# Performance work log

Measured on AMD Instinct MI355X. Metric: run time of the kernel, lower is better.

Reference implementation:

```python
import math
import jax, jax.numpy as jnp
import numpy as np

BATCH = 2048
LATENT = 64
BETA = 6.0
LOG_2PI = math.log(2.0 * math.pi)


def setup_inputs() -> dict:
    key = jax.random.key(0)
    k1, k2, k3 = jax.random.split(key, 3)
    z = jax.random.normal(k1, (BATCH, LATENT), dtype=jnp.float32)
    z_mean = jax.random.normal(k2, (BATCH, LATENT), dtype=jnp.float32)
    z_logvar = jax.random.normal(k3, (BATCH, LATENT), dtype=jnp.float32)
    return {"z": z, "z_mean": z_mean, "z_logvar": z_logvar}


def _gaussian_log_density(samples, mean, log_var):
    # elementwise Gaussian log-density, broadcasts to [B, B, L]
    inv_sigma = jnp.exp(-log_var)
    tmp = samples - mean
    return -0.5 * (tmp * tmp * inv_sigma + log_var + LOG_2PI)


def _total_correlation(z, z_mean, z_logvar):
    # log q(z_i | x_j) per-dim: [B, B, L]
    log_qz_prob = _gaussian_log_density(z[:, None, :], z_mean[None, :, :], z_logvar[None, :, :])
    # log prod_l (1/B) sum_j q(z_l | x_j)  (constants dropped as in original)
    log_qz_product = jnp.sum(jax.scipy.special.logsumexp(log_qz_prob, axis=1), axis=1)  # [B]
    # log (1/B) sum_j q(z | x_j)
    log_qz = jax.scipy.special.logsumexp(jnp.sum(log_qz_prob, axis=2), axis=1)  # [B]
    return jnp.mean(log_qz - log_qz_product)


def _gaussian_kl(z_mean, z_logvar):
    # standard KL(q(z|x) || N(0, I)), mean over batch
    return 0.5 * jnp.mean(
        jnp.sum(jnp.square(z_mean) + jnp.exp(z_logvar) - z_logvar - 1.0, axis=1)
    )


def reference(z, z_mean, z_logvar):
    kl_loss = _gaussian_kl(z_mean, z_logvar)
    tc = (BETA - 1.0) * _total_correlation(z, z_mean, z_logvar)
    return tc + kl_loss
```

## Files before the change

kernel.cpp:

```cpp
#include <hip/hip_runtime.h>
#include <math.h>

#define BATCH 2048
#define LATENT 64
#define LOG_2PI 1.8378770664093453f
#define BETA_M1 5.0f
#define LN2 0.69314718055994530942f
#define C2 (-0.72134752044448170368f)
#define EXP2F __builtin_amdgcn_exp2f
#define LOG2F __builtin_amdgcn_logf

#define OFF_VT   0
#define OFF_TCE  (128*BATCH)
#define OFF_UP   (OFF_TCE + 64*BATCH)
#define OFF_CE   (OFF_UP + 128*BATCH)
#define OFF_KLP  (OFF_CE + BATCH)
#define OFF_RMP  (OFF_KLP + BATCH)
#define OFF_RSP  (OFF_RMP + 8*BATCH)
#define OFF_PART (OFF_RSP + 8*BATCH)
#define OFF_SM   (OFF_PART + 16)

__global__ __launch_bounds__(256) void precompute_kernel(const float* __restrict__ z,
                                                         const float* __restrict__ zm,
                                                         const float* __restrict__ zlv,
                                                         float* __restrict__ ws) {
    __shared__ float Tz[16][65], Tm[16][65], Tlv[16][65];
    __shared__ float CEp[16][16], KLp[16][16];
    int t = threadIdx.x, lane = t & 63, w = t >> 6;
    int j0 = blockIdx.x * 16;

    #pragma unroll
    for (int p = 0; p < 4; ++p) {
        int jr = p * 4 + w;
        int idx = (j0 + jr) * LATENT + lane;
        Tz[jr][lane]  = z[idx];
        Tm[jr][lane]  = zm[idx];
        Tlv[jr][lane] = zlv[idx];
    }
    if (blockIdx.x == 0 && t < 16) ws[OFF_PART + t] = 0.0f;
    __syncthreads();

    int jl = t & 15, lg = t >> 4;
    int j = j0 + jl;
    float ce_acc = 0.0f, kl_acc = 0.0f;
    #pragma unroll
    for (int q = 0; q < 4; ++q) {
        int l = q * 16 + lg;
        float zv = Tz[jl][l];
        float m  = Tm[jl][l];
        float lv = Tlv[jl][l];
        float iv  = __expf(-lv);
        float civ = C2 * iv;
        float miv = m * iv;
        float cmv = C2 * miv;
        float cev = C2 * fmaf(m, miv, lv + LOG_2PI);
        ws[OFF_VT  + (2*l)   * BATCH + j] = civ;
        ws[OFF_VT  + (2*l+1) * BATCH + j] = cmv;
        ws[OFF_TCE + l       * BATCH + j] = cev;
        ws[OFF_UP  + (2*l)   * BATCH + j] = zv * zv;
        ws[OFF_UP  + (2*l+1) * BATCH + j] = -2.0f * zv;
        ce_acc += cev;
        kl_acc += fmaf(m, m, __expf(lv)) - lv - 1.0f;
    }
    CEp[lg][jl] = ce_acc;
    KLp[lg][jl] = kl_acc;
    __syncthreads();
    if (t < 16) {
        float ce = 0.0f, kl = 0.0f;
        #pragma unroll
        for (int g = 0; g < 16; ++g) { ce += CEp[g][t]; kl += KLp[g][t]; }
        ws[OFF_CE  + j0 + t] = ce;
        ws[OFF_KLP + j0 + t] = kl;
    }
}


__device__ __forceinline__ void dim_part(float* __restrict__ ws, int bx, int t,
                                         float (*Dred)[64]) {
    int l = bx >> 5, ic = bx & 31;
    int i0 = ic * 64;
    int ig = t & 7, js = t >> 3;
    int ib = i0 + ig * 8;

    const float* __restrict__ up0 = ws + OFF_UP + (2*l)   * BATCH + ib;
    const float* __restrict__ up1 = ws + OFF_UP + (2*l+1) * BATCH + ib;
    float4 za = *(const float4*)(up0);
    float4 zb = *(const float4*)(up0 + 4);
    float4 na = *(const float4*)(up1);
    float4 nb = *(const float4*)(up1 + 4);
    float z2[8] = {za.x, za.y, za.z, za.w, zb.x, zb.y, zb.z, zb.w};
    float n2[8] = {na.x, na.y, na.z, na.w, nb.x, nb.y, nb.z, nb.w};

    const float4* __restrict__ pc4 = (const float4*)(ws + OFF_VT  + (2*l)   * BATCH + js * 64);
    const float4* __restrict__ pm4 = (const float4*)(ws + OFF_VT  + (2*l+1) * BATCH + js * 64);
    const float4* __restrict__ pe4 = (const float4*)(ws + OFF_TCE + l       * BATCH + js * 64);

    float s[8] = {0.f, 0.f, 0.f, 0.f, 0.f, 0.f, 0.f, 0.f};

    #pragma unroll 4
    for (int q = 0; q < 16; ++q) {
        float4 cc = pc4[q], mm = pm4[q], ee = pe4[q];
        #pragma unroll
        for (int k = 0; k < 8; ++k) {
            s[k] += EXP2F(fmaf(z2[k], cc.x, fmaf(n2[k], mm.x, ee.x)));
            s[k] += EXP2F(fmaf(z2[k], cc.y, fmaf(n2[k], mm.y, ee.y)));
            s[k] += EXP2F(fmaf(z2[k], cc.z, fmaf(n2[k], mm.z, ee.z)));
            s[k] += EXP2F(fmaf(z2[k], cc.w, fmaf(n2[k], mm.w, ee.w)));
        }
    }

    #pragma unroll
    for (int off = 8; off < 64; off <<= 1) {
        #pragma unroll
        for (int k = 0; k < 8; ++k)
            s[k] += __shfl_xor(s[k], off, 64);
    }
    int lane = t & 63, w = t >> 6;
    if (lane < 8) {
        #pragma unroll
        for (int k = 0; k < 8; ++k) Dred[w][lane * 8 + k] = s[k];
    }
    __syncthreads();
    if (t < 64) {
        float v = Dred[0][t] + Dred[1][t] + Dred[2][t] + Dred[3][t];
        ws[OFF_SM + l * BATCH + i0 + t] = v;
    }
    __syncthreads();
}

__device__ __forceinline__ void row_part(float* __restrict__ ws, int bx, int t,
                                         float* __restrict__ Ups,
                                         float (*RMs)[4], float (*RSs)[4]) {
    int ig = bx >> 3, jq = bx & 7;
    int i0 = ig * 8;
    int j  = jq * 256 + t;

    #pragma unroll
    for (int p = 0; p < 4; ++p) {
        int f = t + 256 * p;
        Ups[f] = ws[OFF_UP + (f >> 3) * BATCH + i0 + (f & 7)];
    }
    __syncthreads();

    float r[8];
    #pragma unroll
    for (int i = 0; i < 8; ++i) r[i] = 0.0f;

    const float* __restrict__ Vt = ws + OFF_VT;
    for (int l = 0; l < LATENT; ++l) {
        float v0 = Vt[(2*l)   * BATCH + j];
        float v1 = Vt[(2*l+1) * BATCH + j];
        const float* __restrict__ ua = Ups + (2*l)   * 8;
        const float* __restrict__ ub = Ups + (2*l+1) * 8;
        #pragma unroll
        for (int i = 0; i < 8; ++i)
            r[i] = fmaf(ua[i], v0, fmaf(ub[i], v1, r[i]));
    }

    float ce = ws[OFF_CE + j];
    int lane = t & 63, w = t >> 6;
    #pragma unroll
    for (int i = 0; i < 8; ++i) {
        float M = r[i] + ce;
        float S = 1.0f;
        #pragma unroll
        for (int off = 32; off > 0; off >>= 1) {
            float Mo = __shfl_xor(M, off, 64);
            float So = __shfl_xor(S, off, 64);
            float mn = fmaxf(M, Mo);
            S = S * EXP2F(M - mn) + So * EXP2F(Mo - mn);
            M = mn;
        }
        if (lane == 0) { RMs[i][w] = M; RSs[i][w] = S; }
    }
    __syncthreads();
    if (t < 8) {
        float M = RMs[t][0], S = RSs[t][0];
        #pragma unroll
        for (int w2 = 1; w2 < 4; ++w2) {
            float Mo = RMs[t][w2], So = RSs[t][w2];
            float mn = fmaxf(M, Mo);
            S = S * EXP2F(M - mn) + So * EXP2F(Mo - mn);
            M = mn;
        }
        ws[OFF_RMP + jq * BATCH + i0 + t] = M;
        ws[OFF_RSP + jq * BATCH + i0 + t] = S;
    }
    __syncthreads();
}

__global__ __launch_bounds__(256, 4) void main_kernel(float* __restrict__ ws) {
    __shared__ float Ups[1024];
    __shared__ float Dred[4][64];
    __shared__ float RMs[8][4], RSs[8][4];
    int bx = blockIdx.x, t = threadIdx.x;
    if (((bx >> 8) & 1) == 0) {
        dim_part(ws, bx, t, Dred);
        row_part(ws, bx, t, Ups, RMs, RSs);
    } else {
        row_part(ws, bx, t, Ups, RMs, RSs);
        dim_part(ws, bx, t, Dred);
    }
}

__global__ __launch_bounds__(256) void finalize_kernel(float* __restrict__ ws,
                                                       float* __restrict__ out) {
    __shared__ float s_tc[256];
    __shared__ float s_kl[256];
    int t = threadIdx.x;
    int gid = blockIdx.x * 256 + t;

    float acc = 0.0f, kl = 0.0f;
    #pragma unroll
    for (int k = 0; k < 4; ++k) {
        float s = ws[OFF_SM + gid + 32768 * k];
        acc -= LOG2F(s);
    }

    if (gid < BATCH) {
        int i = gid;
        float M = ws[OFF_RMP + i];
        float S = ws[OFF_RSP + i];
        #pragma unroll
        for (int q = 1; q < 8; ++q) {
            float Mo = ws[OFF_RMP + q * BATCH + i];
            float So = ws[OFF_RSP + q * BATCH + i];
            float mn = fmaxf(M, Mo);
            S = S * EXP2F(M - mn) + So * EXP2F(Mo - mn);
            M = mn;
        }
        acc += M + LOG2F(S);
        kl = ws[OFF_KLP + i];
    }

    s_tc[t] = acc; s_kl[t] = kl;
    __syncthreads();
    for (int s2 = 128; s2 > 0; s2 >>= 1) {
        if (t < s2) { s_tc[t] += s_tc[t + s2]; s_kl[t] += s_kl[t + s2]; }
        __syncthreads();
    }
    if (t == 0) {
        atomicAdd(&ws[OFF_PART + 0], s_tc[0]);
        atomicAdd(&ws[OFF_PART + 1], s_kl[0]);
        __threadfence();
        unsigned int old = atomicAdd((unsigned int*)(ws + OFF_PART + 2), 1u);
        if (old == 127u) {
            float tc  = atomicAdd(&ws[OFF_PART + 0], 0.0f);
            float kl2 = atomicAdd(&ws[OFF_PART + 1], 0.0f);
            out[0] = BETA_M1 * (LN2 * tc / (float)BATCH) + 0.5f * (kl2 / (float)BATCH);
        }
    }
}

extern "C" void kernel_launch(void* const* d_in, const int* in_sizes, int n_in,
                              void* d_out, int out_size, void* d_ws, size_t ws_size,
                              hipStream_t stream) {
    const float* z        = (const float*)d_in[0];
    const float* z_mean   = (const float*)d_in[1];
    const float* z_logvar = (const float*)d_in[2];
    float* out = (float*)d_out;
    float* ws  = (float*)d_ws;

    precompute_kernel<<<128, 256, 0, stream>>>(z, z_mean, z_logvar, ws);
    main_kernel<<<2048, 256, 0, stream>>>(ws);
    finalize_kernel<<<128, 256, 0, stream>>>(ws, out);
}
```

Baseline: 127.0 us.

## Register-block row logsumexp over 4 columns per thread and split work blocks

The row part now has each thread handle 4 consecutive j columns with float4 loads and an 8x4 register accumulator tile. This cuts row blocks from 2048 to 512 and the partial max/sum slices from 8 to 2. The main kernel no longer runs both a dim-part and a row-part in every block: 2560 blocks are interleaved as 4 dim blocks per row block, and trailing syncthreads are dropped. Finalize merges only 2 partials. The aim is fewer redundant Ups loads and less reduction work, in exchange for higher register pressure in the row part and possible load imbalance between the two block types.

```diff
diff --git a/kernel.cpp b/kernel.cpp
--- a/kernel.cpp
+++ b/kernel.cpp
@@ -16,8 +16,8 @@
 #define OFF_CE   (OFF_UP + 128*BATCH)
 #define OFF_KLP  (OFF_CE + BATCH)
 #define OFF_RMP  (OFF_KLP + BATCH)
-#define OFF_RSP  (OFF_RMP + 8*BATCH)
-#define OFF_PART (OFF_RSP + 8*BATCH)
+#define OFF_RSP  (OFF_RMP + 2*BATCH)
+#define OFF_PART (OFF_RSP + 2*BATCH)
 #define OFF_SM   (OFF_PART + 16)
 
 __global__ __launch_bounds__(256) void precompute_kernel(const float* __restrict__ z,
@@ -75,9 +75,9 @@
 }
 
 
-__device__ __forceinline__ void dim_part(float* __restrict__ ws, int bx, int t,
+__device__ __forceinline__ void dim_part(float* __restrict__ ws, int d, int t,
                                          float (*Dred)[64]) {
-    int l = bx >> 5, ic = bx & 31;
+    int l = d >> 5, ic = d & 31;
     int i0 = ic * 64;
     int ig = t & 7, js = t >> 3;
     int ib = i0 + ig * 8;
@@ -125,15 +125,14 @@
         float v = Dred[0][t] + Dred[1][t] + Dred[2][t] + Dred[3][t];
         ws[OFF_SM + l * BATCH + i0 + t] = v;
     }
-    __syncthreads();
-}
-
-__device__ __forceinline__ void row_part(float* __restrict__ ws, int bx, int t,
+}
+
+__device__ __forceinline__ void row_part(float* __restrict__ ws, int r, int t,
                                          float* __restrict__ Ups,
                                          float (*RMs)[4], float (*RSs)[4]) {
-    int ig = bx >> 3, jq = bx & 7;
+    int ig = r >> 1, jh = r & 1;
     int i0 = ig * 8;
-    int j  = jq * 256 + t;
+    int jb = jh * 1024 + 4 * t;
 
     #pragma unroll
     for (int p = 0; p < 4; ++p) {
@@ -142,27 +141,36 @@
     }
     __syncthreads();
 
-    float r[8];
-    #pragma unroll
-    for (int i = 0; i < 8; ++i) r[i] = 0.0f;
+    float acc[8][4];
+    #pragma unroll
+    for (int i = 0; i < 8; ++i)
+        acc[i][0] = acc[i][1] = acc[i][2] = acc[i][3] = 0.0f;
 
     const float* __restrict__ Vt = ws + OFF_VT;
     for (int l = 0; l < LATENT; ++l) {
-        float v0 = Vt[(2*l)   * BATCH + j];
-        float v1 = Vt[(2*l+1) * BATCH + j];
+        float4 v0 = *(const float4*)(Vt + (2*l)   * BATCH + jb);
+        float4 v1 = *(const float4*)(Vt + (2*l+1) * BATCH + jb);
         const float* __restrict__ ua = Ups + (2*l)   * 8;
         const float* __restrict__ ub = Ups + (2*l+1) * 8;
         #pragma unroll
-        for (int i = 0; i < 8; ++i)
-            r[i] = fmaf(ua[i], v0, fmaf(ub[i], v1, r[i]));
-    }
-
-    float ce = ws[OFF_CE + j];
+        for (int i = 0; i < 8; ++i) {
+            float a = ua[i], b = ub[i];
+            acc[i][0] = fmaf(a, v0.x, fmaf(b, v1.x, acc[i][0]));
+            acc[i][1] = fmaf(a, v0.y, fmaf(b, v1.y, acc[i][1]));
+            acc[i][2] = fmaf(a, v0.z, fmaf(b, v1.z, acc[i][2]));
+            acc[i][3] = fmaf(a, v0.w, fmaf(b, v1.w, acc[i][3]));
+        }
+    }
+
+    float4 ce4 = *(const float4*)(ws + OFF_CE + jb);
     int lane = t & 63, w = t >> 6;
     #pragma unroll
     for (int i = 0; i < 8; ++i) {
-        float M = r[i] + ce;
-        float S = 1.0f;
+        float rc0 = acc[i][0] + ce4.x, rc1 = acc[i][1] + ce4.y;
+        float rc2 = acc[i][2] + ce4.z, rc3 = acc[i][3] + ce4.w;
+        float M = fmaxf(fmaxf(rc0, rc1), fmaxf(rc2, rc3));
+        float S = EXP2F(rc0 - M) + EXP2F(rc1 - M)
+                + EXP2F(rc2 - M) + EXP2F(rc3 - M);
         #pragma unroll
         for (int off = 32; off > 0; off >>= 1) {
             float Mo = __shfl_xor(M, off, 64);
@@ -183,10 +191,9 @@
             S = S * EXP2F(M - mn) + So * EXP2F(Mo - mn);
             M = mn;
         }
-        ws[OFF_RMP + jq * BATCH + i0 + t] = M;
-        ws[OFF_RSP + jq * BATCH + i0 + t] = S;
-    }
-    __syncthreads();
+        ws[OFF_RMP + jh * BATCH + i0 + t] = M;
+        ws[OFF_RSP + jh * BATCH + i0 + t] = S;
+    }
 }
 
 __global__ __launch_bounds__(256, 4) void main_kernel(float* __restrict__ ws) {
@@ -194,13 +201,9 @@
     __shared__ float Dred[4][64];
     __shared__ float RMs[8][4], RSs[8][4];
     int bx = blockIdx.x, t = threadIdx.x;
-    if (((bx >> 8) & 1) == 0) {
-        dim_part(ws, bx, t, Dred);
-        row_part(ws, bx, t, Ups, RMs, RSs);
-    } else {
-        row_part(ws, bx, t, Ups, RMs, RSs);
-        dim_part(ws, bx, t, Dred);
-    }
+    int m = bx % 5, q = bx / 5;
+    if (m < 4) dim_part(ws, q * 4 + m, t, Dred);
+    else       row_part(ws, q, t, Ups, RMs, RSs);
 }
 
 __global__ __launch_bounds__(256) void finalize_kernel(float* __restrict__ ws,
@@ -219,17 +222,10 @@
 
     if (gid < BATCH) {
         int i = gid;
-        float M = ws[OFF_RMP + i];
-        float S = ws[OFF_RSP + i];
-        #pragma unroll
-        for (int q = 1; q < 8; ++q) {
-            float Mo = ws[OFF_RMP + q * BATCH + i];
-            float So = ws[OFF_RSP + q * BATCH + i];
-            float mn = fmaxf(M, Mo);
-            S = S * EXP2F(M - mn) + So * EXP2F(Mo - mn);
-            M = mn;
-        }
-        acc += M + LOG2F(S);
+        float M0 = ws[OFF_RMP + i], M1 = ws[OFF_RMP + BATCH + i];
+        float S0 = ws[OFF_RSP + i], S1 = ws[OFF_RSP + BATCH + i];
+        float mn = fmaxf(M0, M1);
+        acc += mn + LOG2F(S0 * EXP2F(M0 - mn) + S1 * EXP2F(M1 - mn));
         kl = ws[OFF_KLP + i];
     }
 
@@ -262,6 +258,6 @@
     float* ws  = (float*)d_ws;
 
     precompute_kernel<<<128, 256, 0, stream>>>(z, z_mean, z_logvar, ws);
-    main_kernel<<<2048, 256, 0, stream>>>(ws);
+    main_kernel<<<2560, 256, 0, stream>>>(ws);
     finalize_kernel<<<128, 256, 0, stream>>>(ws, out);
 }
```

Result: faster. 123.8 us (-2.5%).
